# Kernel optimization log

Measured on AMD Instinct MI355X. Metric: run time of the kernel, lower is better.

Reference implementation:

```python
import jax, jax.numpy as jnp
import numpy as np
import math

B, IN_CH, OUT_CH, STYLE, KS, DIL, L = 16, 128, 256, 512, 3, 1, 16384


def setup_inputs() -> dict:
    key = jax.random.key(0)
    ks = jax.random.split(key, 6)
    return {
        "x": jax.random.normal(ks[0], (B, IN_CH, L), jnp.float32),
        "style": jax.random.normal(ks[1], (B, STYLE), jnp.float32),
        "conv_weight": jax.random.normal(ks[2], (1, OUT_CH, IN_CH, KS), jnp.float32),
        "mod_weight": jax.random.normal(ks[3], (IN_CH, STYLE), jnp.float32),
        "mod_bias": jnp.ones((IN_CH,), jnp.float32),  # bias_init=1 in EqualLinear
        "out_v": jax.random.normal(ks[4], (IN_CH, OUT_CH // 2, 1), jnp.float32),
        "out_g": jax.random.uniform(ks[5], (IN_CH, 1, 1), jnp.float32, 0.5, 1.5),
        "out_bias": jnp.zeros((IN_CH,), jnp.float32),
    }


def reference(x, style, conv_weight, mod_weight, mod_bias, out_v, out_g, out_bias):
    scale_conv = 1.0 / math.sqrt(IN_CH * KS ** 2)  # fan_in = in_channel * k**2
    scale_mod = 1.0 / math.sqrt(STYLE)             # EqualLinear scale, lr_mul=1

    # modulation: EqualLinear(style_dim -> in_channel)
    s = style @ (mod_weight * scale_mod).T + mod_bias            # [B, I]

    # per-sample modulated + demodulated conv weight
    w = scale_conv * conv_weight * s[:, None, :, None]           # [B, O, I, K]
    demod = jax.lax.rsqrt(jnp.sum(w * w, axis=(2, 3)) + 1e-8)    # [B, O]
    w = w * demod[:, :, None, None]

    # grouped (groups=batch) dilated conv1d == per-sample conv via unfold + einsum
    pad = (KS - 1) // 2 * DIL
    xp = jnp.pad(x, ((0, 0), (0, 0), (pad, pad)))
    patches = jnp.stack([xp[:, :, k * DIL:k * DIL + L] for k in range(KS)], axis=2)  # [B, I, K, L]
    out = jnp.einsum('boik,bikl->bol', w, patches)               # [B, O, L]

    # gated tanh-sigmoid
    xa, xb = jnp.split(out, 2, axis=1)
    g = jnp.tanh(xa) * jax.nn.sigmoid(xb)                        # [B, O//2, L]

    # weight-normed 1x1 conv (dim=0: norm over in_ch and k per out channel)
    vnorm = jnp.sqrt(jnp.sum(out_v * out_v, axis=(1, 2), keepdims=True))
    w1 = (out_g * out_v / vnorm)[:, :, 0]                        # [R, O//2]
    y = jnp.einsum('oc,bcl->bol', w1, g) + out_bias[None, :, None]

    return (y + x) * math.sqrt(0.5)
```

## Files before the change

kernel.cpp:

```cpp
#include <hip/hip_runtime.h>
#include <hip/hip_bf16.h>
#include <math.h>

typedef float f32x4 __attribute__((ext_vector_type(4)));
typedef short bh8  __attribute__((ext_vector_type(8)));
typedef unsigned int u32x4 __attribute__((ext_vector_type(4)));

#define B_   16
#define IC   128
#define OC   256
#define RC   128
#define STY  512
#define KS_  3
#define LL   16384
#define LT   128

#define WS_S_OFF   0
#define WS_W_OFF   8192
#define WS_W1_OFF  (8192 + 3145728)

#define SMEM_BYTES 33280

__device__ __forceinline__ unsigned short f2b(float f) {
    union { float f; unsigned int u; } z; z.f = f;
    unsigned int u = z.u;
    return (unsigned short)((u + 0x7fffu + ((u >> 16) & 1u)) >> 16);
}

__device__ __forceinline__ float b2f(unsigned int u16) {
    union { unsigned int u; float f; } z; z.u = u16 << 16;
    return z.f;
}

__device__ __forceinline__ unsigned int pack2bf(float a, float b) {
    __hip_bfloat162 p = __float22bfloat162_rn(make_float2(a, b));
    return *(unsigned int*)&p;
}

__global__ void k_style(const float* __restrict__ style, const float* __restrict__ mw,
                        const float* __restrict__ mb, float* __restrict__ s_out) {
    const int b = blockIdx.x, i = threadIdx.x;
    const float4* st = (const float4*)(style + b * STY);
    const float4* w  = (const float4*)(mw + (size_t)i * STY);
    float acc = 0.f;
#pragma unroll 4
    for (int j = 0; j < STY / 4; ++j) {
        float4 a = st[j], c = w[j];
        acc += a.x * c.x + a.y * c.y + a.z * c.z + a.w * c.w;
    }
    s_out[b * IC + i] = acc * 0.044194173824159216f + mb[i];
}

__global__ void k_modw(const float* __restrict__ cw, const float* __restrict__ s,
                       unsigned short* __restrict__ wbf) {
    const int o = blockIdx.x, b = blockIdx.y, i = threadIdx.x;
    const float sv = s[b * IC + i] * 0.029462782549439476f;
    const float w0 = cw[(o * IC + i) * KS_ + 0] * sv;
    const float w1 = cw[(o * IC + i) * KS_ + 1] * sv;
    const float w2 = cw[(o * IC + i) * KS_ + 2] * sv;
    float ss = w0 * w0 + w1 * w1 + w2 * w2;
    for (int off = 32; off; off >>= 1) ss += __shfl_down(ss, off, 64);
    __shared__ float red[2];
    if ((i & 63) == 0) red[i >> 6] = ss;
    __syncthreads();
    const float d = rsqrtf(red[0] + red[1] + 1e-8f);
    unsigned short* dst = wbf + ((size_t)b * OC + o) * 384 + i;
    dst[0]   = f2b(w0 * d);
    dst[128] = f2b(w1 * d);
    dst[256] = f2b(w2 * d);
}

__global__ void k_w1(const float* __restrict__ v, const float* __restrict__ g,
                     unsigned short* __restrict__ w1bf) {
    const int o = blockIdx.x, c = threadIdx.x;
    const float vv = v[o * RC + c];
    float ss = vv * vv;
    for (int off = 32; off; off >>= 1) ss += __shfl_down(ss, off, 64);
    __shared__ float red[2];
    if ((c & 63) == 0) red[c >> 6] = ss;
    __syncthreads();
    w1bf[o * RC + c] = f2b(g[o] * vv * rsqrtf(red[0] + red[1]) * 0.70710678118654752f);
}

__global__ __launch_bounds__(512, 4) void k_main(
    const float* __restrict__ x, const unsigned short* __restrict__ wbf,
    const unsigned short* __restrict__ w1bf, const float* __restrict__ obias,
    float* __restrict__ out) {
    __shared__ alignas(16) char smem[SMEM_BYTES];

    const int t = threadIdx.x;
    const int lane = t & 63, wv = t >> 6;
    const int lm = lane & 15, kg = lane >> 4;
    const int c0 = wv * 16 + kg * 4;

    const int lid = blockIdx.x;
    const int swz = (lid & 7) * 256 + (lid >> 3);
    const int b  = swz >> 7;
    const int l0 = (swz & 127) * LT;

    const float* xb = x + (size_t)b * IC * LL + l0;

    {
        const int chb = wv * 16;
#pragma unroll
        for (int p = 0; p < 2; ++p) {
            const int pos = lane + p * 64;
            const int row = pos + 1;
#pragma unroll
            for (int h = 0; h < 2; ++h) {
                float xv[8];
#pragma unroll
                for (int c = 0; c < 8; ++c)
                    xv[c] = xb[(size_t)(chb + h * 8 + c) * LL + pos];
                u32x4 wvec;
                wvec.x = pack2bf(xv[0], xv[1]);
                wvec.y = pack2bf(xv[2], xv[3]);
                wvec.z = pack2bf(xv[4], xv[5]);
                wvec.w = pack2bf(xv[6], xv[7]);
                *(u32x4*)(smem + row * 256 +
                          (((chb + h * 8) * 2) ^ ((row & 15) << 4))) = wvec;
            }
        }
    }
    if (t < 128) {
        const float* hx = x + ((size_t)b * IC + t) * LL;
        float lf = (l0 > 0) ? hx[l0 - 1] : 0.f;
        float rt = (l0 + LT < LL) ? hx[l0 + LT] : 0.f;
        *(unsigned short*)(smem + 0 * 256 + ((t * 2) ^ ((0 & 15) << 4)))     = f2b(lf);
        *(unsigned short*)(smem + 129 * 256 + ((t * 2) ^ ((129 & 15) << 4))) = f2b(rt);
    }
    __syncthreads();

    f32x4 acc[2][8];
#pragma unroll
    for (int m = 0; m < 2; ++m)
#pragma unroll
        for (int nt = 0; nt < 8; ++nt) acc[m][nt] = (f32x4){0.f, 0.f, 0.f, 0.f};

    const unsigned short* wa = wbf + ((size_t)b * OC + wv * 16 + lm) * 384 + kg * 8;
    const unsigned short* wb2 = wa + 128 * 384;

    bh8 ca0 = *(const bh8*)(wa + 0);
    bh8 ca1 = *(const bh8*)(wb2 + 0);
#pragma unroll
    for (int kc = 0; kc < 12; ++kc) {
        bh8 na0 = ca0, na1 = ca1;
        if (kc < 11) {
            const int nkoff = ((kc + 1) >> 2) * 128 + ((kc + 1) & 3) * 32;
            na0 = *(const bh8*)(wa + nkoff);
            na1 = *(const bh8*)(wb2 + nkoff);
        }
        const int tap = kc >> 2;
        const int icb = (kc & 3) * 32;
#pragma unroll
        for (int nt = 0; nt < 8; ++nt) {
            const int lr = nt * 16 + lm + tap;
            const bh8 bf = *(const bh8*)(smem + lr * 256 +
                                         (((icb + kg * 8) * 2) ^ ((lr & 15) << 4)));
            acc[0][nt] = __builtin_amdgcn_mfma_f32_16x16x32_bf16(ca0, bf, acc[0][nt], 0, 0, 0);
            acc[1][nt] = __builtin_amdgcn_mfma_f32_16x16x32_bf16(ca1, bf, acc[1][nt], 0, 0, 0);
        }
        ca0 = na0; ca1 = na1;
    }

    const int myc = wv * 16 + lm;
    const float bias = obias[myc];
    f32x4 cin[8];
#pragma unroll
    for (int m = 0; m < 8; ++m) {
#pragma unroll
        for (int j = 0; j < 4; ++j) {
            const int row = m * 16 + kg * 4 + j + 1;
            const unsigned short xu = *(const unsigned short*)(
                smem + row * 256 + ((myc * 2) ^ ((row & 15) << 4)));
            cin[m][j] = (b2f(xu) + bias) * 0.70710678118654752f;
        }
    }

    const unsigned short* w1p = w1bf + (size_t)myc * RC + kg * 8;
    bh8 w1f[4];
#pragma unroll
    for (int kc = 0; kc < 4; ++kc) w1f[kc] = *(const bh8*)(w1p + kc * 32);

    unsigned long long gw[8];
#pragma unroll
    for (int nt = 0; nt < 8; ++nt) {
        float g4[4];
#pragma unroll
        for (int j = 0; j < 4; ++j) {
            const float xa = acc[0][nt][j], xg = acc[1][nt][j];
            const float th = 1.f - 2.f * __builtin_amdgcn_rcpf(__expf(2.f * xa) + 1.f);
            const float sg = __builtin_amdgcn_rcpf(1.f + __expf(-xg));
            g4[j] = th * sg;
        }
        gw[nt] = (unsigned long long)pack2bf(g4[0], g4[1]) |
                 ((unsigned long long)pack2bf(g4[2], g4[3]) << 32);
    }
    __syncthreads();

#pragma unroll
    for (int nt = 0; nt < 8; ++nt) {
        const int n = nt * 16 + lm;
        *(unsigned long long*)(smem + n * 256 + ((c0 * 2) ^ ((n & 15) << 4))) = gw[nt];
    }
    __syncthreads();

    float* orow = out + ((size_t)b * IC + myc) * LL + l0 + kg * 4;
#pragma unroll
    for (int m = 0; m < 8; ++m) {
        f32x4 acc2 = cin[m];
#pragma unroll
        for (int kc = 0; kc < 4; ++kc) {
            const int n = m * 16 + lm;
            const bh8 ga = *(const bh8*)(smem + n * 256 +
                                         (((kc * 32 + kg * 8) * 2) ^ ((n & 15) << 4)));
            acc2 = __builtin_amdgcn_mfma_f32_16x16x32_bf16(ga, w1f[kc], acc2, 0, 0, 0);
        }
        float4 ov;
        ov.x = acc2[0]; ov.y = acc2[1]; ov.z = acc2[2]; ov.w = acc2[3];
        *(float4*)(orow + m * 16) = ov;
    }
}

extern "C" void kernel_launch(void* const* d_in, const int* in_sizes, int n_in,
                              void* d_out, int out_size, void* d_ws, size_t ws_size,
                              hipStream_t stream) {
    (void)in_sizes; (void)n_in; (void)out_size; (void)ws_size;
    const float* x        = (const float*)d_in[0];
    const float* style    = (const float*)d_in[1];
    const float* conv_w   = (const float*)d_in[2];
    const float* mod_w    = (const float*)d_in[3];
    const float* mod_b    = (const float*)d_in[4];
    const float* out_v    = (const float*)d_in[5];
    const float* out_g    = (const float*)d_in[6];
    const float* out_bias = (const float*)d_in[7];
    float* out = (float*)d_out;

    float* s_buf = (float*)((char*)d_ws + WS_S_OFF);
    unsigned short* wbf  = (unsigned short*)((char*)d_ws + WS_W_OFF);
    unsigned short* w1bf = (unsigned short*)((char*)d_ws + WS_W1_OFF);

    k_style<<<dim3(B_), 128, 0, stream>>>(style, mod_w, mod_b, s_buf);
    k_modw<<<dim3(OC, B_), 128, 0, stream>>>(conv_w, s_buf, wbf);
    k_w1<<<dim3(RC), 128, 0, stream>>>(out_v, out_g, w1bf);
    k_main<<<dim3(B_ * LL / LT), 512, 0, stream>>>(x, wbf, w1bf, out_bias, out);
}
```

Measured before the change: 123.9 us.

## Retile conv MFMA to 4x4 wave tiles and pack residual in bf16 registers

```diff
diff --git a/kernel.cpp b/kernel.cpp
--- a/kernel.cpp
+++ b/kernel.cpp
@@ -91,7 +91,9 @@
     const int t = threadIdx.x;
     const int lane = t & 63, wv = t >> 6;
     const int lm = lane & 15, kg = lane >> 4;
-    const int c0 = wv * 16 + kg * 4;
+
+    const int w2 = wv >> 1;
+    const int nb = (wv & 1) * 64;
 
     const int lid = blockIdx.x;
     const int swz = (lid & 7) * 256 + (lid >> 3);
@@ -131,84 +133,91 @@
     }
     __syncthreads();
 
-    f32x4 acc[2][8];
-#pragma unroll
-    for (int m = 0; m < 2; ++m)
-#pragma unroll
-        for (int nt = 0; nt < 8; ++nt) acc[m][nt] = (f32x4){0.f, 0.f, 0.f, 0.f};
-
-    const unsigned short* wa = wbf + ((size_t)b * OC + wv * 16 + lm) * 384 + kg * 8;
-    const unsigned short* wb2 = wa + 128 * 384;
-
-    bh8 ca0 = *(const bh8*)(wa + 0);
-    bh8 ca1 = *(const bh8*)(wb2 + 0);
+    f32x4 acc[4][4];
+#pragma unroll
+    for (int mt = 0; mt < 4; ++mt)
+#pragma unroll
+        for (int nt = 0; nt < 4; ++nt) acc[mt][nt] = (f32x4){0.f, 0.f, 0.f, 0.f};
+
+    const unsigned short* wa0 = wbf + ((size_t)b * OC + 32 * w2 + lm) * 384 + kg * 8;
+
 #pragma unroll
     for (int kc = 0; kc < 12; ++kc) {
-        bh8 na0 = ca0, na1 = ca1;
-        if (kc < 11) {
-            const int nkoff = ((kc + 1) >> 2) * 128 + ((kc + 1) & 3) * 32;
-            na0 = *(const bh8*)(wa + nkoff);
-            na1 = *(const bh8*)(wb2 + nkoff);
-        }
         const int tap = kc >> 2;
         const int icb = (kc & 3) * 32;
-#pragma unroll
-        for (int nt = 0; nt < 8; ++nt) {
-            const int lr = nt * 16 + lm + tap;
+        const int koff = tap * 128 + icb;
+        bh8 af[4];
+        af[0] = *(const bh8*)(wa0 + koff);
+        af[1] = *(const bh8*)(wa0 + 16 * 384 + koff);
+        af[2] = *(const bh8*)(wa0 + 128 * 384 + koff);
+        af[3] = *(const bh8*)(wa0 + 144 * 384 + koff);
+#pragma unroll
+        for (int nt = 0; nt < 4; ++nt) {
+            const int lr = nb + nt * 16 + lm + tap;
             const bh8 bf = *(const bh8*)(smem + lr * 256 +
                                          (((icb + kg * 8) * 2) ^ ((lr & 15) << 4)));
-            acc[0][nt] = __builtin_amdgcn_mfma_f32_16x16x32_bf16(ca0, bf, acc[0][nt], 0, 0, 0);
-            acc[1][nt] = __builtin_amdgcn_mfma_f32_16x16x32_bf16(ca1, bf, acc[1][nt], 0, 0, 0);
-        }
-        ca0 = na0; ca1 = na1;
+#pragma unroll
+            for (int mt = 0; mt < 4; ++mt)
+                acc[mt][nt] = __builtin_amdgcn_mfma_f32_16x16x32_bf16(af[mt], bf, acc[mt][nt], 0, 0, 0);
+        }
     }
 
     const int myc = wv * 16 + lm;
-    const float bias = obias[myc];
-    f32x4 cin[8];
+    unsigned int xp[16];
 #pragma unroll
     for (int m = 0; m < 8; ++m) {
 #pragma unroll
-        for (int j = 0; j < 4; ++j) {
-            const int row = m * 16 + kg * 4 + j + 1;
-            const unsigned short xu = *(const unsigned short*)(
-                smem + row * 256 + ((myc * 2) ^ ((row & 15) << 4)));
-            cin[m][j] = (b2f(xu) + bias) * 0.70710678118654752f;
-        }
-    }
+        for (int jp = 0; jp < 2; ++jp) {
+            const int r0 = m * 16 + kg * 4 + jp * 2 + 1;
+            const int r1 = r0 + 1;
+            const unsigned int x0 = *(const unsigned short*)(
+                smem + r0 * 256 + ((myc * 2) ^ ((r0 & 15) << 4)));
+            const unsigned int x1 = *(const unsigned short*)(
+                smem + r1 * 256 + ((myc * 2) ^ ((r1 & 15) << 4)));
+            xp[m * 2 + jp] = x0 | (x1 << 16);
+        }
+    }
+
+    unsigned long long gw[2][4];
+#pragma unroll
+    for (int mt = 0; mt < 2; ++mt) {
+#pragma unroll
+        for (int nt = 0; nt < 4; ++nt) {
+            float g4[4];
+#pragma unroll
+            for (int j = 0; j < 4; ++j) {
+                const float xa = acc[mt][nt][j], xg = acc[mt + 2][nt][j];
+                const float th = 1.f - 2.f * __builtin_amdgcn_rcpf(__expf(2.f * xa) + 1.f);
+                const float sg = __builtin_amdgcn_rcpf(1.f + __expf(-xg));
+                g4[j] = th * sg;
+            }
+            gw[mt][nt] = (unsigned long long)pack2bf(g4[0], g4[1]) |
+                         ((unsigned long long)pack2bf(g4[2], g4[3]) << 32);
+        }
+    }
+    __syncthreads();
+
+#pragma unroll
+    for (int mt = 0; mt < 2; ++mt) {
+#pragma unroll
+        for (int nt = 0; nt < 4; ++nt) {
+            const int n = nb + nt * 16 + lm;
+            const int cc = 32 * w2 + 16 * mt + kg * 4;
+            *(unsigned long long*)(smem + n * 256 + ((cc * 2) ^ ((n & 15) << 4))) = gw[mt][nt];
+        }
+    }
+    __syncthreads();
 
     const unsigned short* w1p = w1bf + (size_t)myc * RC + kg * 8;
     bh8 w1f[4];
 #pragma unroll
     for (int kc = 0; kc < 4; ++kc) w1f[kc] = *(const bh8*)(w1p + kc * 32);
 
-    unsigned long long gw[8];
-#pragma unroll
-    for (int nt = 0; nt < 8; ++nt) {
-        float g4[4];
-#pragma unroll
-        for (int j = 0; j < 4; ++j) {
-            const float xa = acc[0][nt][j], xg = acc[1][nt][j];
-            const float th = 1.f - 2.f * __builtin_amdgcn_rcpf(__expf(2.f * xa) + 1.f);
-            const float sg = __builtin_amdgcn_rcpf(1.f + __expf(-xg));
-            g4[j] = th * sg;
-        }
-        gw[nt] = (unsigned long long)pack2bf(g4[0], g4[1]) |
-                 ((unsigned long long)pack2bf(g4[2], g4[3]) << 32);
-    }
-    __syncthreads();
-
-#pragma unroll
-    for (int nt = 0; nt < 8; ++nt) {
-        const int n = nt * 16 + lm;
-        *(unsigned long long*)(smem + n * 256 + ((c0 * 2) ^ ((n & 15) << 4))) = gw[nt];
-    }
-    __syncthreads();
-
+    const float bias = obias[myc];
     float* orow = out + ((size_t)b * IC + myc) * LL + l0 + kg * 4;
 #pragma unroll
     for (int m = 0; m < 8; ++m) {
-        f32x4 acc2 = cin[m];
+        f32x4 acc2 = (f32x4){0.f, 0.f, 0.f, 0.f};
 #pragma unroll
         for (int kc = 0; kc < 4; ++kc) {
             const int n = m * 16 + lm;
@@ -217,7 +226,10 @@
             acc2 = __builtin_amdgcn_mfma_f32_16x16x32_bf16(ga, w1f[kc], acc2, 0, 0, 0);
         }
         float4 ov;
-        ov.x = acc2[0]; ov.y = acc2[1]; ov.z = acc2[2]; ov.w = acc2[3];
+        ov.x = acc2[0] + (b2f(xp[m * 2] & 0xffffu)       + bias) * 0.70710678118654752f;
+        ov.y = acc2[1] + (b2f(xp[m * 2] >> 16)           + bias) * 0.70710678118654752f;
+        ov.z = acc2[2] + (b2f(xp[m * 2 + 1] & 0xffffu)   + bias) * 0.70710678118654752f;
+        ov.w = acc2[3] + (b2f(xp[m * 2 + 1] >> 16)       + bias) * 0.70710678118654752f;
         *(float4*)(orow + m * 16) = ov;
     }
 }
```

Measured after the change: 167.9 us. +35.5%, slower.
